# Performance work log

Hardware: AMD Instinct MI355X
Metric: run time of the kernel (lower is better)

Reference implementation:

```python
import jax, jax.numpy as jnp
import numpy as np

# ---- GridEncoder hyperparams (from init_kwargs) ----
B = 1048576
D = 3           # input_dim
NL = 16         # num_levels
C = 2           # level_dim
HBASE = 16      # base_resolution
LOG2_HASH = 19  # log2_hashmap_size
DESIRED = 2048  # desired_resolution
PLS = float(np.exp2(np.log2(DESIRED / HBASE) / (NL - 1)))  # per_level_scale recomputed as in __init__
PRIMES = (np.uint32(1), np.uint32(2654435761), np.uint32(805459861))  # instant-ngp spatial hash primes


def _level_config():
    # Mirrors the offsets construction in GridEncoder.__init__ (align_corners=False)
    max_params = 2 ** LOG2_HASH
    sides, sizes, offs = [], [], [0]
    for i in range(NL):
        side = int(np.ceil(HBASE * PLS ** i)) + 1  # grid side length (+1 because align_corners=False)
        params = min(max_params, side ** D)
        params = int(np.ceil(params / 8) * 8)      # align to 8
        sides.append(side)
        sizes.append(params)
        offs.append(offs[-1] + params)
    return sides, sizes, offs

SIDES, SIZES, OFFS = _level_config()
TOTAL_PARAMS = OFFS[-1]  # 6119864

# 2^D corner offsets in {0,1}^D, shape [8, D]
_CORNERS = np.stack(np.meshgrid(*([np.arange(2)] * D), indexing='ij'), -1).reshape(-1, D)


def _encode(inputs, embeddings):
    """Multi-resolution hash grid encode: inputs [B,D] in [0,1] -> [B, NL*C]."""
    corners_u = jnp.asarray(_CORNERS, dtype=jnp.uint32)        # [8, D]
    corners_f = jnp.asarray(_CORNERS, dtype=inputs.dtype)      # [8, D]
    outs = []
    for l in range(NL):  # fixed small loop over resolution levels
        side, size, off = SIDES[l], SIZES[l], OFFS[l]
        scale = HBASE * PLS ** l - 1.0
        pos = inputs * scale + 0.5                 # align_corners=False offset
        pos_floor = jnp.floor(pos)
        frac = pos - pos_floor                     # [B, D]
        pg = pos_floor.astype(jnp.uint32)          # [B, D], non-negative
        corner = jnp.minimum(pg[:, None, :] + corners_u[None], np.uint32(side - 1))  # [B, 8, D]
        # trilinear weights: frac if corner bit set else (1-frac), product over D
        w = jnp.prod(frac[:, None, :] * corners_f[None] + (1 - frac[:, None, :]) * (1 - corners_f[None]), axis=-1)  # [B, 8]
        if side ** D > size:
            # hashed level: xor of coord * prime (uint32 wraparound)
            idx = (corner[..., 0] * PRIMES[0]) ^ (corner[..., 1] * PRIMES[1]) ^ (corner[..., 2] * PRIMES[2])
        else:
            # dense level: linear (tiled) index
            idx = corner[..., 0] + corner[..., 1] * np.uint32(side) + corner[..., 2] * np.uint32(side * side)
        idx = (idx % np.uint32(size)).astype(jnp.int32) + off      # [B, 8]
        feat = embeddings[idx]                     # gather corner features [B, 8, C]
        outs.append(jnp.sum(w[..., None] * feat, axis=1))          # [B, C]
    # matches outputs.permute(1,0,2).reshape(B, L*C): levels concatenated per point
    return jnp.concatenate(outs, axis=-1)


def setup_inputs() -> dict:
    key = jax.random.key(0)
    k1, k2 = jax.random.split(key)
    inputs = jax.random.uniform(k1, (B, D), dtype=jnp.float32)
    # torch-ngp style init: uniform(-1e-4, 1e-4)
    embeddings = jax.random.uniform(k2, (TOTAL_PARAMS, C), jnp.float32, -1e-4, 1e-4)
    return {"inputs": inputs, "embeddings": embeddings}


def reference(inputs, embeddings):
    return _encode(inputs, embeddings)
```

## Files before the change

### kernel.cpp

```cpp
#include <hip/hip_runtime.h>
#include <cstdint>
#include <cmath>

#define NLVL 16
#define NDENSE 5

typedef float v2f __attribute__((ext_vector_type(2)));
typedef float v4f __attribute__((ext_vector_type(4)));
typedef float v4f8 __attribute__((ext_vector_type(4), aligned(8)));

struct Params {
    float    scale[NLVL];
    uint32_t side[NLVL];
    uint32_t offset[NLVL];
    uint32_t hashed[NLVL];
};

struct DenseParams {
    float    scale[NDENSE];
    uint32_t side[NDENSE];
    uint32_t offset[NDENSE];
};

__device__ __forceinline__ uint32_t umin32(uint32_t a, uint32_t b) { return a < b ? a : b; }

__device__ __forceinline__ void pair_load(const float* __restrict__ embf,
                                          uint32_t ia, uint32_t ib,
                                          v2f& va, v2f& vb) {
    const v4f q = *(const v4f*)(embf + 2u * (ia & ~1u));
    v2f lo; lo.x = q.x; lo.y = q.y;
    v2f hi; hi.x = q.z; hi.y = q.w;
    va = (ia & 1u) ? hi : lo;
    if ((ia ^ ib) > 1u) {
        vb = *(const v2f*)(embf + 2u * ib);
    } else {
        vb = (ib & 1u) ? hi : lo;
    }
}

__device__ __forceinline__ void dense_pair_load(const float* __restrict__ embf,
                                                uint32_t ia, uint32_t clamped,
                                                v2f& va, v2f& vb) {
    const v4f8 q = *(const v4f8*)(embf + 2u * ia);
    va.x = q.x; va.y = q.y;
    v2f hi; hi.x = q.z; hi.y = q.w;
    vb = clamped ? va : hi;
}

__global__ __launch_bounds__(256) void hash_level_kernel(
    const float* __restrict__ in, const float* __restrict__ embf,
    v2f* __restrict__ wsl, float scale, uint32_t side, uint32_t off, uint32_t npts)
{
    const uint32_t i = blockIdx.x * 256u + threadIdx.x;
    if (i >= npts) return;
    const float x = in[3u * i + 0u];
    const float y = in[3u * i + 1u];
    const float z = in[3u * i + 2u];

    float p0 = x * scale + 0.5f, p1 = y * scale + 0.5f, p2 = z * scale + 0.5f;
    float fl0 = floorf(p0), fl1 = floorf(p1), fl2 = floorf(p2);
    float f0 = p0 - fl0, f1 = p1 - fl1, f2 = p2 - fl2;
    uint32_t g0 = (uint32_t)fl0, g1 = (uint32_t)fl1, g2 = (uint32_t)fl2;

    const uint32_t smax = side - 1u;
    uint32_t c0a = umin32(g0, smax), c0b = umin32(g0 + 1u, smax);
    uint32_t c1a = umin32(g1, smax), c1b = umin32(g1 + 1u, smax);
    uint32_t c2a = umin32(g2, smax), c2b = umin32(g2 + 1u, smax);

    const uint32_t h1a = c1a * 2654435761u, h1b = c1b * 2654435761u;
    const uint32_t h2a = c2a * 805459861u,  h2b = c2b * 805459861u;
    const uint32_t idx0 = ((c0a ^ h1a ^ h2a) & 0x7FFFFu) + off;
    const uint32_t idx1 = ((c0a ^ h1a ^ h2b) & 0x7FFFFu) + off;
    const uint32_t idx2 = ((c0a ^ h1b ^ h2a) & 0x7FFFFu) + off;
    const uint32_t idx3 = ((c0a ^ h1b ^ h2b) & 0x7FFFFu) + off;
    const uint32_t idx4 = ((c0b ^ h1a ^ h2a) & 0x7FFFFu) + off;
    const uint32_t idx5 = ((c0b ^ h1a ^ h2b) & 0x7FFFFu) + off;
    const uint32_t idx6 = ((c0b ^ h1b ^ h2a) & 0x7FFFFu) + off;
    const uint32_t idx7 = ((c0b ^ h1b ^ h2b) & 0x7FFFFu) + off;

    v2f v0, v1, v2, v3, v4, v5, v6, v7;
    pair_load(embf, idx0, idx4, v0, v4);
    pair_load(embf, idx1, idx5, v1, v5);
    pair_load(embf, idx2, idx6, v2, v6);
    pair_load(embf, idx3, idx7, v3, v7);

    const float w0a = 1.0f - f0, w0b = f0;
    const float w1a = 1.0f - f1, w1b = f1;
    const float w2a = 1.0f - f2, w2b = f2;
    v2f r = (w0a * w1a * w2a) * v0 + (w0a * w1a * w2b) * v1
          + (w0a * w1b * w2a) * v2 + (w0a * w1b * w2b) * v3
          + (w0b * w1a * w2a) * v4 + (w0b * w1a * w2b) * v5
          + (w0b * w1b * w2a) * v6 + (w0b * w1b * w2b) * v7;
    __builtin_nontemporal_store(r, wsl + i);
}

__global__ __launch_bounds__(256) void finalize_kernel(
    const float* __restrict__ in, const float* __restrict__ embf,
    const v2f* __restrict__ ws, float* __restrict__ out,
    uint32_t npts, DenseParams P)
{
    __shared__ float lds[256 * 33];
    const uint32_t t = threadIdx.x;
    const uint32_t i = blockIdx.x * 256u + t;

    const float x = in[3u * i + 0u];
    const float y = in[3u * i + 1u];
    const float z = in[3u * i + 2u];
    float* row = lds + t * 33u;

    #pragma unroll
    for (int l = 0; l < NDENSE; ++l) {
        const float scale = P.scale[l];
        const uint32_t side = P.side[l];
        const uint32_t off  = P.offset[l];

        float p0 = x * scale + 0.5f, p1 = y * scale + 0.5f, p2 = z * scale + 0.5f;
        float fl0 = floorf(p0), fl1 = floorf(p1), fl2 = floorf(p2);
        float f0 = p0 - fl0, f1 = p1 - fl1, f2 = p2 - fl2;
        uint32_t g0 = (uint32_t)fl0, g1 = (uint32_t)fl1, g2 = (uint32_t)fl2;

        const uint32_t smax = side - 1u;
        uint32_t c0a = umin32(g0, smax);
        const uint32_t clamped = (c0a == smax) ? 1u : 0u;
        uint32_t c1a = umin32(g1, smax), c1b = umin32(g1 + 1u, smax);
        uint32_t c2a = umin32(g2, smax), c2b = umin32(g2 + 1u, smax);

        const uint32_t s2 = side * side;
        const uint32_t b1a = c1a * side, b1b = c1b * side;
        const uint32_t b2a = c2a * s2,   b2b = c2b * s2;

        v2f v0, v1, v2, v3, v4, v5, v6, v7;
        dense_pair_load(embf, c0a + b1a + b2a + off, clamped, v0, v4);
        dense_pair_load(embf, c0a + b1a + b2b + off, clamped, v1, v5);
        dense_pair_load(embf, c0a + b1b + b2a + off, clamped, v2, v6);
        dense_pair_load(embf, c0a + b1b + b2b + off, clamped, v3, v7);

        const float w0a = 1.0f - f0, w0b = f0;
        const float w1a = 1.0f - f1, w1b = f1;
        const float w2a = 1.0f - f2, w2b = f2;
        v2f r = (w0a * w1a * w2a) * v0 + (w0a * w1a * w2b) * v1
              + (w0a * w1b * w2a) * v2 + (w0a * w1b * w2b) * v3
              + (w0b * w1a * w2a) * v4 + (w0b * w1a * w2b) * v5
              + (w0b * w1b * w2a) * v6 + (w0b * w1b * w2b) * v7;
        row[2 * l]     = r.x;
        row[2 * l + 1] = r.y;
    }

    #pragma unroll
    for (int l = NDENSE; l < NLVL; ++l) {
        v2f r = __builtin_nontemporal_load(ws + (size_t)(l - NDENSE) * npts + i);
        row[2 * l]     = r.x;
        row[2 * l + 1] = r.y;
    }

    __syncthreads();

    float* obase = out + (size_t)blockIdx.x * 256u * 32u;
    #pragma unroll
    for (int k = 0; k < 8; ++k) {
        const uint32_t f = (uint32_t)k * 1024u + t * 4u;
        const uint32_t p = f >> 5, c = f & 31u;
        const float* src = lds + p * 33u + c;
        v4f q; q.x = src[0]; q.y = src[1]; q.z = src[2]; q.w = src[3];
        __builtin_nontemporal_store(q, (v4f*)(obase + f));
    }
}

__global__ __launch_bounds__(256) void grid_encode_mono(
    const float* __restrict__ in, const float* __restrict__ emb,
    float* __restrict__ out, uint32_t npts, Params P)
{
    const uint32_t i = blockIdx.x * 256u + threadIdx.x;
    if (i >= npts) return;
    const float x = in[3u * i + 0u], y = in[3u * i + 1u], z = in[3u * i + 2u];
    const v2f* e2 = (const v2f*)emb;
    float* outp = out + (size_t)i * 32u;

    #pragma unroll 1
    for (int l = 0; l < NLVL; ++l) {
        const float scale = P.scale[l];
        const uint32_t side = P.side[l], off = P.offset[l], hashed = P.hashed[l];
        float p0 = x * scale + 0.5f, p1 = y * scale + 0.5f, p2 = z * scale + 0.5f;
        float fl0 = floorf(p0), fl1 = floorf(p1), fl2 = floorf(p2);
        float f0 = p0 - fl0, f1 = p1 - fl1, f2 = p2 - fl2;
        uint32_t g0 = (uint32_t)fl0, g1 = (uint32_t)fl1, g2 = (uint32_t)fl2;
        const uint32_t smax = side - 1u;
        uint32_t c0a = umin32(g0, smax), c0b = umin32(g0 + 1u, smax);
        uint32_t c1a = umin32(g1, smax), c1b = umin32(g1 + 1u, smax);
        uint32_t c2a = umin32(g2, smax), c2b = umin32(g2 + 1u, smax);
        uint32_t idx0, idx1, idx2, idx3, idx4, idx5, idx6, idx7;
        if (hashed) {
            const uint32_t h1a = c1a * 2654435761u, h1b = c1b * 2654435761u;
            const uint32_t h2a = c2a * 805459861u,  h2b = c2b * 805459861u;
            idx0 = ((c0a ^ h1a ^ h2a) & 0x7FFFFu) + off;
            idx1 = ((c0a ^ h1a ^ h2b) & 0x7FFFFu) + off;
            idx2 = ((c0a ^ h1b ^ h2a) & 0x7FFFFu) + off;
            idx3 = ((c0a ^ h1b ^ h2b) & 0x7FFFFu) + off;
            idx4 = ((c0b ^ h1a ^ h2a) & 0x7FFFFu) + off;
            idx5 = ((c0b ^ h1a ^ h2b) & 0x7FFFFu) + off;
            idx6 = ((c0b ^ h1b ^ h2a) & 0x7FFFFu) + off;
            idx7 = ((c0b ^ h1b ^ h2b) & 0x7FFFFu) + off;
        } else {
            const uint32_t s2 = side * side;
            const uint32_t b1a = c1a * side, b1b = c1b * side;
            const uint32_t b2a = c2a * s2,   b2b = c2b * s2;
            idx0 = (c0a + b1a + b2a) + off; idx1 = (c0a + b1a + b2b) + off;
            idx2 = (c0a + b1b + b2a) + off; idx3 = (c0a + b1b + b2b) + off;
            idx4 = (c0b + b1a + b2a) + off; idx5 = (c0b + b1a + b2b) + off;
            idx6 = (c0b + b1b + b2a) + off; idx7 = (c0b + b1b + b2b) + off;
        }
        const v2f v0 = e2[idx0], v1 = e2[idx1], v2 = e2[idx2], v3 = e2[idx3];
        const v2f v4 = e2[idx4], v5 = e2[idx5], v6 = e2[idx6], v7 = e2[idx7];
        const float w0a = 1.0f - f0, w0b = f0;
        const float w1a = 1.0f - f1, w1b = f1;
        const float w2a = 1.0f - f2, w2b = f2;
        v2f r = (w0a*w1a*w2a) * v0 + (w0a*w1a*w2b) * v1 + (w0a*w1b*w2a) * v2 + (w0a*w1b*w2b) * v3
              + (w0b*w1a*w2a) * v4 + (w0b*w1a*w2b) * v5 + (w0b*w1b*w2a) * v6 + (w0b*w1b*w2b) * v7;
        *(v2f*)(outp + 2 * l) = r;
    }
}

extern "C" void kernel_launch(void* const* d_in, const int* in_sizes, int n_in,
                              void* d_out, int out_size, void* d_ws, size_t ws_size,
                              hipStream_t stream) {
    const float* inputs = (const float*)d_in[0];
    const float* emb    = (const float*)d_in[1];
    float* out          = (float*)d_out;

    Params P;
    DenseParams DP;
    const double PLS = exp2(log2(2048.0 / 16.0) / 15.0);
    uint64_t off = 0;
    for (int l = 0; l < NLVL; ++l) {
        const double s = 16.0 * pow(PLS, (double)l);
        const uint32_t side = (uint32_t)ceil(s) + 1u;
        const uint64_t s3 = (uint64_t)side * side * side;
        uint64_t params = s3 < (1ull << 19) ? s3 : (1ull << 19);
        params = (params + 7ull) / 8ull * 8ull;
        P.scale[l]  = (float)(s - 1.0);
        P.side[l]   = side;
        P.offset[l] = (uint32_t)off;
        P.hashed[l] = (s3 > params) ? 1u : 0u;
        if (l < NDENSE) { DP.scale[l] = P.scale[l]; DP.side[l] = P.side[l]; DP.offset[l] = P.offset[l]; }
        off += params;
    }

    const uint32_t npts = (uint32_t)(in_sizes[0] / 3);
    const uint32_t nblk = (npts + 255u) / 256u;
    const size_t ws_needed = (size_t)(NLVL - NDENSE) * npts * sizeof(v2f);

    if (ws_size >= ws_needed && (npts % 256u) == 0u) {
        v2f* ws = (v2f*)d_ws;
        for (int l = NDENSE; l < NLVL; ++l) {
            hipLaunchKernelGGL(hash_level_kernel, dim3(nblk), dim3(256), 0, stream,
                               inputs, emb, ws + (size_t)(l - NDENSE) * npts,
                               P.scale[l], P.side[l], P.offset[l], npts);
        }
        hipLaunchKernelGGL(finalize_kernel, dim3(nblk), dim3(256), 0, stream,
                           inputs, emb, ws, out, npts, DP);
    } else {
        hipLaunchKernelGGL(grid_encode_mono, dim3(nblk), dim3(256), 0, stream,
                           inputs, emb, out, npts, P);
    }
}
```

Measured before the change: 472.2 us.

## Stage first two dense level tables in LDS and enlarge finalize blocks

The finalize kernel now uses 1024-thread blocks with dynamic shared memory. Each block copies the embedding tables of the first two dense levels (about 150 KB) into LDS and serves those corner lookups from LDS instead of global memory. Per-point results are held in registers and only staged through LDS afterwards for the coalesced transposed store. The cost is a full table copy per block, extra barriers, a very large LDS footprint that limits residency to about one block per CU, and higher register pressure from the 32-float result array.

Measured after the change: 467.0 us. Within noise of the previous version (-1.1%).

```diff
diff --git a/kernel.cpp b/kernel.cpp
--- a/kernel.cpp
+++ b/kernel.cpp
@@ -4,6 +4,10 @@
 
 #define NLVL 16
 #define NDENSE 5
+#define FBLK 1024u
+#define TAB_ENTRIES 18744u
+#define LDS_FLOATS 37504u
+#define LDS_BYTES (LDS_FLOATS * 4u)
 
 typedef float v2f __attribute__((ext_vector_type(2)));
 typedef float v4f __attribute__((ext_vector_type(4)));
@@ -94,19 +98,32 @@
     __builtin_nontemporal_store(r, wsl + i);
 }
 
-__global__ __launch_bounds__(256) void finalize_kernel(
+__global__ __launch_bounds__(1024, 4) void finalize_kernel(
     const float* __restrict__ in, const float* __restrict__ embf,
     const v2f* __restrict__ ws, float* __restrict__ out,
     uint32_t npts, DenseParams P)
 {
-    __shared__ float lds[256 * 33];
+    extern __shared__ float lds[];
     const uint32_t t = threadIdx.x;
-    const uint32_t i = blockIdx.x * 256u + t;
+    const uint32_t i = blockIdx.x * FBLK + t;
+
+    {
+        const v4f* src4 = (const v4f*)embf;
+        v4f* dst4 = (v4f*)lds;
+        #pragma unroll
+        for (uint32_t j = 0; j < 10; ++j) {
+            const uint32_t k = j * FBLK + t;
+            if (k < LDS_FLOATS / 4u) dst4[k] = src4[k];
+        }
+    }
 
     const float x = in[3u * i + 0u];
     const float y = in[3u * i + 1u];
     const float z = in[3u * i + 2u];
-    float* row = lds + t * 33u;
+
+    __syncthreads();
+
+    float res[32];
 
     #pragma unroll
     for (int l = 0; l < NDENSE; ++l) {
@@ -126,14 +143,27 @@
         uint32_t c2a = umin32(g2, smax), c2b = umin32(g2 + 1u, smax);
 
         const uint32_t s2 = side * side;
-        const uint32_t b1a = c1a * side, b1b = c1b * side;
-        const uint32_t b2a = c2a * s2,   b2b = c2b * s2;
+        const uint32_t ia0 = c0a + c1a * side + c2a * s2 + off;
+        const uint32_t ia1 = c0a + c1a * side + c2b * s2 + off;
+        const uint32_t ia2 = c0a + c1b * side + c2a * s2 + off;
+        const uint32_t ia3 = c0a + c1b * side + c2b * s2 + off;
 
         v2f v0, v1, v2, v3, v4, v5, v6, v7;
-        dense_pair_load(embf, c0a + b1a + b2a + off, clamped, v0, v4);
-        dense_pair_load(embf, c0a + b1a + b2b + off, clamped, v1, v5);
-        dense_pair_load(embf, c0a + b1b + b2a + off, clamped, v2, v6);
-        dense_pair_load(embf, c0a + b1b + b2b + off, clamped, v3, v7);
+        if (l < 2) {
+            v0 = *(const v2f*)(lds + 2u * ia0);
+            v4 = clamped ? v0 : *(const v2f*)(lds + 2u * ia0 + 2u);
+            v1 = *(const v2f*)(lds + 2u * ia1);
+            v5 = clamped ? v1 : *(const v2f*)(lds + 2u * ia1 + 2u);
+            v2 = *(const v2f*)(lds + 2u * ia2);
+            v6 = clamped ? v2 : *(const v2f*)(lds + 2u * ia2 + 2u);
+            v3 = *(const v2f*)(lds + 2u * ia3);
+            v7 = clamped ? v3 : *(const v2f*)(lds + 2u * ia3 + 2u);
+        } else {
+            dense_pair_load(embf, ia0, clamped, v0, v4);
+            dense_pair_load(embf, ia1, clamped, v1, v5);
+            dense_pair_load(embf, ia2, clamped, v2, v6);
+            dense_pair_load(embf, ia3, clamped, v3, v7);
+        }
 
         const float w0a = 1.0f - f0, w0b = f0;
         const float w1a = 1.0f - f1, w1b = f1;
@@ -142,23 +172,29 @@
               + (w0a * w1b * w2a) * v2 + (w0a * w1b * w2b) * v3
               + (w0b * w1a * w2a) * v4 + (w0b * w1a * w2b) * v5
               + (w0b * w1b * w2a) * v6 + (w0b * w1b * w2b) * v7;
-        row[2 * l]     = r.x;
-        row[2 * l + 1] = r.y;
+        res[2 * l]     = r.x;
+        res[2 * l + 1] = r.y;
     }
 
     #pragma unroll
     for (int l = NDENSE; l < NLVL; ++l) {
         v2f r = __builtin_nontemporal_load(ws + (size_t)(l - NDENSE) * npts + i);
-        row[2 * l]     = r.x;
-        row[2 * l + 1] = r.y;
+        res[2 * l]     = r.x;
+        res[2 * l + 1] = r.y;
     }
 
     __syncthreads();
-
-    float* obase = out + (size_t)blockIdx.x * 256u * 32u;
+    {
+        float* row = lds + t * 33u;
+        #pragma unroll
+        for (int k = 0; k < 32; ++k) row[k] = res[k];
+    }
+    __syncthreads();
+
+    float* obase = out + (size_t)blockIdx.x * FBLK * 32u;
     #pragma unroll
-    for (int k = 0; k < 8; ++k) {
-        const uint32_t f = (uint32_t)k * 1024u + t * 4u;
+    for (uint32_t k = 0; k < 8; ++k) {
+        const uint32_t f = k * 4096u + t * 4u;
         const uint32_t p = f >> 5, c = f & 31u;
         const float* src = lds + p * 33u + c;
         v4f q; q.x = src[0]; q.y = src[1]; q.z = src[2]; q.w = src[3];
@@ -249,14 +285,20 @@
     const uint32_t nblk = (npts + 255u) / 256u;
     const size_t ws_needed = (size_t)(NLVL - NDENSE) * npts * sizeof(v2f);
 
-    if (ws_size >= ws_needed && (npts % 256u) == 0u) {
+    if (ws_size >= ws_needed && (npts % FBLK) == 0u) {
         v2f* ws = (v2f*)d_ws;
         for (int l = NDENSE; l < NLVL; ++l) {
             hipLaunchKernelGGL(hash_level_kernel, dim3(nblk), dim3(256), 0, stream,
                                inputs, emb, ws + (size_t)(l - NDENSE) * npts,
                                P.scale[l], P.side[l], P.offset[l], npts);
         }
-        hipLaunchKernelGGL(finalize_kernel, dim3(nblk), dim3(256), 0, stream,
+        static bool attr_set = [] {
+            hipFuncSetAttribute(reinterpret_cast<const void*>(finalize_kernel),
+                                hipFuncAttributeMaxDynamicSharedMemorySize, LDS_BYTES);
+            return true;
+        }();
+        (void)attr_set;
+        hipLaunchKernelGGL(finalize_kernel, dim3(npts / FBLK), dim3(FBLK), LDS_BYTES, stream,
                            inputs, emb, ws, out, npts, DP);
     } else {
         hipLaunchKernelGGL(grid_encode_mono, dim3(nblk), dim3(256), 0, stream,
```
